# Kernel tuning notes

Hardware: AMD Instinct MI355X
Metric: run time of the kernel (lower is better)

The kernel has to match this reference:

```python
import jax, jax.numpy as jnp
import numpy as np

B, N, D_MEM, D_HID = 64, 65536, 1024, 1024


def setup_inputs() -> dict:
    key = jax.random.key(0)
    k1, k2, k3 = jax.random.split(key, 3)
    memory_bank = jax.random.normal(k1, (N, D_MEM), dtype=jnp.float32)
    decoder_state = jax.random.normal(k2, (B, D_HID), dtype=jnp.float32)
    # nn.Linear(memory_bank_size -> hidden_size, bias=False): weight [D_HID, D_MEM]
    W = jax.random.normal(k3, (D_HID, D_MEM), dtype=jnp.float32) / np.sqrt(D_MEM)
    # ragged tree sizes summing exactly to N (concrete, built on host)
    rng = np.random.default_rng(0)
    lens = rng.integers(512, 1536, size=B).astype(np.float64)
    lens = np.maximum(1, np.floor(lens * N / lens.sum()).astype(np.int64))
    lens[-1] += N - lens.sum()
    return {
        "memory_bank": memory_bank,
        "decoder_state": decoder_state,
        "W": W,
        "tree_node_num_lst": jnp.asarray(lens, dtype=jnp.int64),
    }


def reference(memory_bank, decoder_state, W, tree_node_num_lst):
    # segment id per node: tree index it belongs to (total_repeat_length keeps it jit-able)
    n_total = memory_bank.shape[0]
    batch = decoder_state.shape[0]
    seg = jnp.repeat(jnp.arange(batch), tree_node_num_lst, total_repeat_length=n_total)  # [N]
    # memory_project: one big GEMM instead of per-tree launches
    enc = memory_bank @ W.T                                  # [N, D_HID]
    # per-node score = <decoder_state[tree], enc[node]>
    scores = jnp.sum(enc * decoder_state[seg], axis=-1)      # [N]
    # segment (per-tree) stable softmax
    m = jax.ops.segment_max(scores, seg, num_segments=batch)  # [B]
    e = jnp.exp(scores - m[seg])                              # [N]
    z = jax.ops.segment_sum(e, seg, num_segments=batch)       # [B]
    attn = e / z[seg]                                         # [N]
    # context = attn-weighted sum of raw memory bank per tree
    context = jax.ops.segment_sum(attn[:, None] * memory_bank, seg, num_segments=batch)  # [B, D_MEM]
    return context
```

## Files before the change

### kernel.cpp

```cpp
#include <hip/hip_runtime.h>
#include <hip/hip_bf16.h>
#include <math.h>

#define B_TREES 64
#define N_NODES 65536
#define D 1024
#define D4 (D/4)

__global__ void offsets_kernel(const int* __restrict__ lens32, int* __restrict__ off) {
    if (threadIdx.x == 0 && blockIdx.x == 0) {
        long long s32 = 0;
        for (int b = 0; b < B_TREES; ++b) s32 += lens32[b];
        const bool is32 = (s32 == (long long)N_NODES);
        int acc = 0;
        off[0] = 0;
        for (int b = 0; b < B_TREES; ++b) {
            int len = is32 ? lens32[b] : (int)(((const long long*)lens32)[b]);
            acc += len;
            off[b + 1] = acc;
        }
    }
}

__global__ void v_kernel(const float* __restrict__ ds, const float* __restrict__ W,
                         float* __restrict__ v) {
    const int m  = blockIdx.x * 256 + threadIdx.x;
    const int b0 = blockIdx.y * 4;
    const int h0 = blockIdx.z * 128;
    float acc[4] = {0.f, 0.f, 0.f, 0.f};
    for (int h = h0; h < h0 + 128; ++h) {
        float wv = W[h * D + m];
        #pragma unroll
        for (int j = 0; j < 4; ++j)
            acc[j] += ds[(b0 + j) * D + h] * wv;
    }
    #pragma unroll
    for (int j = 0; j < 4; ++j)
        atomicAdd(&v[(b0 + j) * D + m], acc[j]);
}

__global__ void scores_kernel(const float4* __restrict__ mb, const float4* __restrict__ v,
                              const int* __restrict__ off, float* __restrict__ scores,
                              int* __restrict__ segarr) {
    const int wave = threadIdx.x >> 6;
    const int lane = threadIdx.x & 63;
    const int node = blockIdx.x * 4 + wave;

    int lo = 0, hi = B_TREES - 1;
    while (lo < hi) {
        int mid = (lo + hi + 1) >> 1;
        if (off[mid] <= node) lo = mid; else hi = mid - 1;
    }

    const float4* mrow = mb + (size_t)node * D4;
    const float4* vrow = v  + (size_t)lo   * D4;
    float acc = 0.f;
    #pragma unroll
    for (int k = 0; k < 4; ++k) {
        float4 a = mrow[k * 64 + lane];
        float4 c = vrow[k * 64 + lane];
        acc += a.x * c.x + a.y * c.y + a.z * c.z + a.w * c.w;
    }
    #pragma unroll
    for (int o = 32; o > 0; o >>= 1) acc += __shfl_down(acc, o, 64);
    if (lane == 0) {
        scores[node] = acc;
        segarr[node] = lo;
    }
}

__global__ void softmax_kernel(const int* __restrict__ off, float* __restrict__ scores) {
    const int b  = blockIdx.x;
    const int s0 = off[b], s1 = off[b + 1];
    const int tid = threadIdx.x;
    __shared__ float red[256];

    float mloc = -INFINITY;
    for (int i = s0 + tid; i < s1; i += 256) mloc = fmaxf(mloc, scores[i]);
    red[tid] = mloc; __syncthreads();
    for (int s = 128; s > 0; s >>= 1) {
        if (tid < s) red[tid] = fmaxf(red[tid], red[tid + s]);
        __syncthreads();
    }
    const float m = red[0]; __syncthreads();

    float zloc = 0.f;
    for (int i = s0 + tid; i < s1; i += 256) zloc += __expf(scores[i] - m);
    red[tid] = zloc; __syncthreads();
    for (int s = 128; s > 0; s >>= 1) {
        if (tid < s) red[tid] += red[tid + s];
        __syncthreads();
    }
    const float inv = 1.f / red[0]; __syncthreads();

    for (int i = s0 + tid; i < s1; i += 256)
        scores[i] = __expf(scores[i] - m) * inv;
}

__global__ void ctx_kernel(const float4* __restrict__ mb, const float* __restrict__ w,
                           const int* __restrict__ segarr, float* __restrict__ out) {
    const int n0 = blockIdx.x * 64;
    const int t  = threadIdx.x;
    float4 acc = make_float4(0.f, 0.f, 0.f, 0.f);
    int cur = segarr[n0];
    for (int i = 0; i < 64; ++i) {
        const int n = n0 + i;
        const int s = segarr[n];
        if (s != cur) {
            float* o = out + (size_t)cur * D + t * 4;
            atomicAdd(o + 0, acc.x); atomicAdd(o + 1, acc.y);
            atomicAdd(o + 2, acc.z); atomicAdd(o + 3, acc.w);
            acc = make_float4(0.f, 0.f, 0.f, 0.f);
            cur = s;
        }
        const float wv = w[n];
        const float4 m4 = mb[(size_t)n * D4 + t];
        acc.x += wv * m4.x; acc.y += wv * m4.y;
        acc.z += wv * m4.z; acc.w += wv * m4.w;
    }
    float* o = out + (size_t)cur * D + t * 4;
    atomicAdd(o + 0, acc.x); atomicAdd(o + 1, acc.y);
    atomicAdd(o + 2, acc.z); atomicAdd(o + 3, acc.w);
}

extern "C" void kernel_launch(void* const* d_in, const int* in_sizes, int n_in,
                              void* d_out, int out_size, void* d_ws, size_t ws_size,
                              hipStream_t stream) {
    const float* mb   = (const float*)d_in[0];
    const float* ds   = (const float*)d_in[1];
    const float* W    = (const float*)d_in[2];
    const int*   lens = (const int*)d_in[3];
    float*       out  = (float*)d_out;

    char* ws = (char*)d_ws;
    int*   off    = (int*)ws;
    float* v      = (float*)(ws + 512);
    float* scores = (float*)(ws + 512 + 64 * D * 4);
    int*   segarr = (int*)  (ws + 512 + 64 * D * 4 + N_NODES * 4);

    hipMemsetAsync(v, 0, 64 * D * sizeof(float), stream);
    hipMemsetAsync(out, 0, B_TREES * D * sizeof(float), stream);

    offsets_kernel<<<1, 64, 0, stream>>>(lens, off);

    {
        dim3 grid(4, 16, 8);
        v_kernel<<<grid, 256, 0, stream>>>(ds, W, v);
    }

    scores_kernel<<<N_NODES / 4, 256, 0, stream>>>(
        (const float4*)mb, (const float4*)v, off, scores, segarr);

    softmax_kernel<<<B_TREES, 256, 0, stream>>>(off, scores);

    ctx_kernel<<<N_NODES / 64, 256, 0, stream>>>(
        (const float4*)mb, scores, segarr, out);
}
```

Baseline: 436.3 us.

## Fuse scores, segment softmax and context into one online-softmax pass over memory bank

Replaces the separate scores, softmax and context kernels with a single chunked kernel. Each 64-node chunk is staged in shared memory once and used both for the dot products and for an online-softmax weighted accumulation. Per-chunk partial max, sum and vector are written to slots, and a small combine kernel rescales and merges them per tree. This avoids reading the 256MB memory bank twice and removes the output atomics, at the cost of extra partial-vector traffic and one more synchronisation per sub-tile. The code assumes each chunk spans at most two trees.

```diff
diff --git a/kernel.cpp b/kernel.cpp
--- a/kernel.cpp
+++ b/kernel.cpp
@@ -1,11 +1,16 @@
 #include <hip/hip_runtime.h>
-#include <hip/hip_bf16.h>
 #include <math.h>
 
 #define B_TREES 64
 #define N_NODES 65536
 #define D 1024
 #define D4 (D/4)
+
+#define CHUNK 64
+#define SUB 8
+#define NSUB (CHUNK/SUB)
+#define NCHUNK (N_NODES/CHUNK)
+#define NSLOT (2*NCHUNK)
 
 __global__ void offsets_kernel(const int* __restrict__ lens32, int* __restrict__ off) {
     if (threadIdx.x == 0 && blockIdx.x == 0) {
@@ -39,88 +44,146 @@
         atomicAdd(&v[(b0 + j) * D + m], acc[j]);
 }
 
-__global__ void scores_kernel(const float4* __restrict__ mb, const float4* __restrict__ v,
-                              const int* __restrict__ off, float* __restrict__ scores,
-                              int* __restrict__ segarr) {
-    const int wave = threadIdx.x >> 6;
-    const int lane = threadIdx.x & 63;
-    const int node = blockIdx.x * 4 + wave;
-
-    int lo = 0, hi = B_TREES - 1;
-    while (lo < hi) {
-        int mid = (lo + hi + 1) >> 1;
-        if (off[mid] <= node) lo = mid; else hi = mid - 1;
-    }
-
-    const float4* mrow = mb + (size_t)node * D4;
-    const float4* vrow = v  + (size_t)lo   * D4;
-    float acc = 0.f;
-    #pragma unroll
-    for (int k = 0; k < 4; ++k) {
-        float4 a = mrow[k * 64 + lane];
-        float4 c = vrow[k * 64 + lane];
-        acc += a.x * c.x + a.y * c.y + a.z * c.z + a.w * c.w;
-    }
-    #pragma unroll
-    for (int o = 32; o > 0; o >>= 1) acc += __shfl_down(acc, o, 64);
-    if (lane == 0) {
-        scores[node] = acc;
-        segarr[node] = lo;
-    }
-}
-
-__global__ void softmax_kernel(const int* __restrict__ off, float* __restrict__ scores) {
-    const int b  = blockIdx.x;
+__global__ __launch_bounds__(256) void fused_kernel(
+    const float4* __restrict__ mb, const float4* __restrict__ v,
+    const int* __restrict__ off,
+    float* __restrict__ m_arr, float* __restrict__ z_arr,
+    int* __restrict__ seg_arr, float4* __restrict__ vec)
+{
+    __shared__ float4 smb[SUB * D4];
+    __shared__ float  ssc[SUB];
+    __shared__ int    sinfo[2];
+
+    const int tid  = threadIdx.x;
+    const int wave = tid >> 6;
+    const int lane = tid & 63;
+    const int c    = blockIdx.x;
+    const int n0   = c * CHUNK;
+
+    if (tid == 0) {
+        int lo = 0, hi = B_TREES - 1;
+        while (lo < hi) { int mid = (lo + hi + 1) >> 1; if (off[mid] <= n0) lo = mid; else hi = mid - 1; }
+        sinfo[0] = lo;
+        const int nxt = off[lo + 1];
+        sinfo[1] = (nxt < n0 + CHUNK) ? nxt : 0x7fffffff;
+    }
+    __syncthreads();
+    const int sa   = sinfo[0];
+    const int cutg = sinfo[1];
+    const bool two = (cutg != 0x7fffffff);
+
+    float  m0 = -INFINITY, z0 = 0.f, m1 = -INFINITY, z1 = 0.f;
+    float4 a0 = make_float4(0.f, 0.f, 0.f, 0.f);
+    float4 a1 = make_float4(0.f, 0.f, 0.f, 0.f);
+
+    float4 vr0, vr1, vr2, vr3;
+    int vcur = -1;
+
+    for (int st = 0; st < NSUB; ++st) {
+        const int nb = n0 + st * SUB;
+        #pragma unroll
+        for (int k = 0; k < SUB; ++k)
+            smb[k * D4 + tid] = mb[(size_t)(nb + k) * D4 + tid];
+        __syncthreads();
+
+        #pragma unroll
+        for (int q = 0; q < 2; ++q) {
+            const int k  = wave * 2 + q;
+            const int sg = (nb + k < cutg) ? sa : sa + 1;
+            if (sg != vcur) {
+                vcur = sg;
+                vr0 = v[(size_t)sg * D4 +   0 + lane];
+                vr1 = v[(size_t)sg * D4 +  64 + lane];
+                vr2 = v[(size_t)sg * D4 + 128 + lane];
+                vr3 = v[(size_t)sg * D4 + 192 + lane];
+            }
+            const float4 b0v = smb[k * D4 +   0 + lane];
+            const float4 b1v = smb[k * D4 +  64 + lane];
+            const float4 b2v = smb[k * D4 + 128 + lane];
+            const float4 b3v = smb[k * D4 + 192 + lane];
+            float acc = b0v.x*vr0.x + b0v.y*vr0.y + b0v.z*vr0.z + b0v.w*vr0.w;
+            acc      += b1v.x*vr1.x + b1v.y*vr1.y + b1v.z*vr1.z + b1v.w*vr1.w;
+            acc      += b2v.x*vr2.x + b2v.y*vr2.y + b2v.z*vr2.z + b2v.w*vr2.w;
+            acc      += b3v.x*vr3.x + b3v.y*vr3.y + b3v.z*vr3.z + b3v.w*vr3.w;
+            #pragma unroll
+            for (int o = 32; o > 0; o >>= 1) acc += __shfl_down(acc, o, 64);
+            if (lane == 0) ssc[k] = acc;
+        }
+        __syncthreads();
+
+        #pragma unroll
+        for (int k = 0; k < SUB; ++k) {
+            const float  s    = ssc[k];
+            const float4 arow = smb[k * D4 + tid];
+            if (nb + k < cutg) {
+                if (s > m0) {
+                    const float sc = __expf(m0 - s);
+                    z0 *= sc; a0.x *= sc; a0.y *= sc; a0.z *= sc; a0.w *= sc;
+                    m0 = s;
+                }
+                const float w = __expf(s - m0);
+                z0 += w;
+                a0.x += w * arow.x; a0.y += w * arow.y; a0.z += w * arow.z; a0.w += w * arow.w;
+            } else {
+                if (s > m1) {
+                    const float sc = __expf(m1 - s);
+                    z1 *= sc; a1.x *= sc; a1.y *= sc; a1.z *= sc; a1.w *= sc;
+                    m1 = s;
+                }
+                const float w = __expf(s - m1);
+                z1 += w;
+                a1.x += w * arow.x; a1.y += w * arow.y; a1.z += w * arow.z; a1.w += w * arow.w;
+            }
+        }
+        __syncthreads();
+    }
+
+    const int slot0 = 2 * c, slot1 = 2 * c + 1;
+    vec[(size_t)slot0 * D4 + tid] = a0;
+    if (tid == 0) { m_arr[slot0] = m0; z_arr[slot0] = z0; seg_arr[slot0] = sa; }
+    if (two) {
+        vec[(size_t)slot1 * D4 + tid] = a1;
+        if (tid == 0) { m_arr[slot1] = m1; z_arr[slot1] = z1; seg_arr[slot1] = sa + 1; }
+    } else if (tid == 0) {
+        seg_arr[slot1] = -1;
+    }
+}
+
+__global__ __launch_bounds__(256) void combine_kernel(
+    const int* __restrict__ off, const float* __restrict__ m_arr,
+    const float* __restrict__ z_arr, const int* __restrict__ seg_arr,
+    const float4* __restrict__ vec, float4* __restrict__ out)
+{
+    const int b = blockIdx.x, t = threadIdx.x;
     const int s0 = off[b], s1 = off[b + 1];
-    const int tid = threadIdx.x;
-    __shared__ float red[256];
-
-    float mloc = -INFINITY;
-    for (int i = s0 + tid; i < s1; i += 256) mloc = fmaxf(mloc, scores[i]);
-    red[tid] = mloc; __syncthreads();
-    for (int s = 128; s > 0; s >>= 1) {
-        if (tid < s) red[tid] = fmaxf(red[tid], red[tid + s]);
-        __syncthreads();
-    }
-    const float m = red[0]; __syncthreads();
-
-    float zloc = 0.f;
-    for (int i = s0 + tid; i < s1; i += 256) zloc += __expf(scores[i] - m);
-    red[tid] = zloc; __syncthreads();
-    for (int s = 128; s > 0; s >>= 1) {
-        if (tid < s) red[tid] += red[tid + s];
-        __syncthreads();
-    }
-    const float inv = 1.f / red[0]; __syncthreads();
-
-    for (int i = s0 + tid; i < s1; i += 256)
-        scores[i] = __expf(scores[i] - m) * inv;
-}
-
-__global__ void ctx_kernel(const float4* __restrict__ mb, const float* __restrict__ w,
-                           const int* __restrict__ segarr, float* __restrict__ out) {
-    const int n0 = blockIdx.x * 64;
-    const int t  = threadIdx.x;
+    const int c0 = s0 / CHUNK, c1 = (s1 - 1) / CHUNK;
+
+    float mseg = -INFINITY;
+    for (int cc = c0; cc <= c1; ++cc) {
+        #pragma unroll
+        for (int j = 0; j < 2; ++j) {
+            const int sl = 2 * cc + j;
+            if (seg_arr[sl] == b) mseg = fmaxf(mseg, m_arr[sl]);
+        }
+    }
+    float zseg = 0.f;
     float4 acc = make_float4(0.f, 0.f, 0.f, 0.f);
-    int cur = segarr[n0];
-    for (int i = 0; i < 64; ++i) {
-        const int n = n0 + i;
-        const int s = segarr[n];
-        if (s != cur) {
-            float* o = out + (size_t)cur * D + t * 4;
-            atomicAdd(o + 0, acc.x); atomicAdd(o + 1, acc.y);
-            atomicAdd(o + 2, acc.z); atomicAdd(o + 3, acc.w);
-            acc = make_float4(0.f, 0.f, 0.f, 0.f);
-            cur = s;
-        }
-        const float wv = w[n];
-        const float4 m4 = mb[(size_t)n * D4 + t];
-        acc.x += wv * m4.x; acc.y += wv * m4.y;
-        acc.z += wv * m4.z; acc.w += wv * m4.w;
-    }
-    float* o = out + (size_t)cur * D + t * 4;
-    atomicAdd(o + 0, acc.x); atomicAdd(o + 1, acc.y);
-    atomicAdd(o + 2, acc.z); atomicAdd(o + 3, acc.w);
+    for (int cc = c0; cc <= c1; ++cc) {
+        #pragma unroll
+        for (int j = 0; j < 2; ++j) {
+            const int sl = 2 * cc + j;
+            if (seg_arr[sl] == b) {
+                const float sc = __expf(m_arr[sl] - mseg);
+                zseg += sc * z_arr[sl];
+                const float4 vv = vec[(size_t)sl * D4 + t];
+                acc.x += sc * vv.x; acc.y += sc * vv.y;
+                acc.z += sc * vv.z; acc.w += sc * vv.w;
+            }
+        }
+    }
+    const float inv = 1.f / zseg;
+    acc.x *= inv; acc.y *= inv; acc.z *= inv; acc.w *= inv;
+    out[(size_t)b * D4 + t] = acc;
 }
 
 extern "C" void kernel_launch(void* const* d_in, const int* in_sizes, int n_in,
@@ -132,14 +195,15 @@
     const int*   lens = (const int*)d_in[3];
     float*       out  = (float*)d_out;
 
-    char* ws = (char*)d_ws;
-    int*   off    = (int*)ws;
-    float* v      = (float*)(ws + 512);
-    float* scores = (float*)(ws + 512 + 64 * D * 4);
-    int*   segarr = (int*)  (ws + 512 + 64 * D * 4 + N_NODES * 4);
+    char*  ws      = (char*)d_ws;
+    int*   off     = (int*)ws;
+    float* v       = (float*)(ws + 512);
+    float* m_arr   = (float*)(ws + 512 + 64 * D * 4);
+    float* z_arr   = m_arr + NSLOT;
+    int*   seg_arr = (int*)(z_arr + NSLOT);
+    float* vec     = (float*)((char*)(seg_arr + NSLOT));
 
     hipMemsetAsync(v, 0, 64 * D * sizeof(float), stream);
-    hipMemsetAsync(out, 0, B_TREES * D * sizeof(float), stream);
 
     offsets_kernel<<<1, 64, 0, stream>>>(lens, off);
 
@@ -148,11 +212,9 @@
         v_kernel<<<grid, 256, 0, stream>>>(ds, W, v);
     }
 
-    scores_kernel<<<N_NODES / 4, 256, 0, stream>>>(
-        (const float4*)mb, (const float4*)v, off, scores, segarr);
-
-    softmax_kernel<<<B_TREES, 256, 0, stream>>>(off, scores);
-
-    ctx_kernel<<<N_NODES / 64, 256, 0, stream>>>(
-        (const float4*)mb, scores, segarr, out);
-}
+    fused_kernel<<<NCHUNK, 256, 0, stream>>>(
+        (const float4*)mb, (const float4*)v, off, m_arr, z_arr, seg_arr, (float4*)vec);
+
+    combine_kernel<<<B_TREES, 256, 0, stream>>>(
+        off, m_arr, z_arr, seg_arr, (const float4*)vec, (float4*)out);
+}
```

After: 406.3 us. 1.07x faster.
